# Performance work log

Hardware: AMD Instinct MI355X
Metric: run time of the kernel (lower is better)

## Reference

```python
import jax, jax.numpy as jnp
import numpy as np

H = 256
L = 3
LN_EPS = 1e-5


def _layernorm(z, g, b):
    mu = jnp.mean(z, axis=-1, keepdims=True)
    var = jnp.mean(jnp.square(z - mu), axis=-1, keepdims=True)
    return (z - mu) / jnp.sqrt(var + LN_EPS) * g + b


def setup_inputs() -> dict:
    key = jax.random.key(0)
    ks = jax.random.split(key, 32)
    B, n = 32, 1024
    N = B * n
    E = 16 * N
    node_in, edge_in = 3, 4
    s = 0.05
    inp = {
        'x': jax.random.normal(ks[0], (N, node_in), jnp.float32),
        'edge_attr': jax.random.normal(ks[1], (E, edge_in), jnp.float32),
        'edge_index': jax.random.randint(ks[2], (2, E), 0, N, jnp.int64),
        'a': jax.random.randint(ks[3], (B, n), 0, 2, jnp.int32),
        # node_proj: Linear(node_in+1 -> H)
        'np_w': jax.random.normal(ks[4], (node_in + 1, H), jnp.float32) * s,
        'np_b': jnp.zeros((H,), jnp.float32),
        # edge_mlp: Linear(edge_in->H), ReLU, Linear(H->H)
        'em_w1': jax.random.normal(ks[5], (edge_in, H), jnp.float32) * s,
        'em_b1': jnp.zeros((H,), jnp.float32),
        'em_w2': jax.random.normal(ks[6], (H, H), jnp.float32) * s,
        'em_b2': jnp.zeros((H,), jnp.float32),
        # per-layer GINEConv internal edge lin (edge_dim=H -> H)
        'lin_w': jax.random.normal(ks[7], (L, H, H), jnp.float32) * s,
        'lin_b': jnp.zeros((L, H), jnp.float32),
        # per-layer GINEConv nn: Linear(H->H), ReLU, Linear(H->H)
        'm_w1': jax.random.normal(ks[8], (L, H, H), jnp.float32) * s,
        'm_b1': jnp.zeros((L, H), jnp.float32),
        'm_w2': jax.random.normal(ks[9], (L, H, H), jnp.float32) * s,
        'm_b2': jnp.zeros((L, H), jnp.float32),
        # per-layer LayerNorm
        'ln_g': jnp.ones((L, H), jnp.float32),
        'ln_b': jnp.zeros((L, H), jnp.float32),
        # head: Linear(H->H), ReLU, Linear(H->1)
        'hd_w1': jax.random.normal(ks[10], (H, H), jnp.float32) * s,
        'hd_b1': jnp.zeros((H,), jnp.float32),
        'hd_w2': jax.random.normal(ks[11], (H, 1), jnp.float32) * s,
        'hd_b2': jnp.zeros((1,), jnp.float32),
    }
    return inp


def reference(x, edge_attr, edge_index, a,
              np_w, np_b, em_w1, em_b1, em_w2, em_b2,
              lin_w, lin_b, m_w1, m_b1, m_w2, m_b2, ln_g, ln_b,
              hd_w1, hd_b1, hd_w2, hd_b2):
    N = x.shape[0]
    B, n = a.shape
    # graphs are packed contiguously: batch = i//n, local = i%n ->
    # a[batch, local] == a.reshape(-1)
    a_s = a.reshape(-1).astype(x.dtype)[:, None]            # [N,1]
    h = jax.nn.relu(jnp.concatenate([x, a_s], -1) @ np_w + np_b)  # [N,H]
    e = jax.nn.relu(edge_attr @ em_w1 + em_b1) @ em_w2 + em_b2    # [E,H]
    src, dst = edge_index[0], edge_index[1]
    for l in range(L):
        e_l = e @ lin_w[l] + lin_b[l]                       # GINEConv edge lin
        msg = jax.nn.relu(h[src] + e_l)                     # [E,H]
        agg = jax.ops.segment_sum(msg, dst, num_segments=N) # scatter-add
        z = h + agg                                          # (1+eps)*h, eps=0
        z = jax.nn.relu(z @ m_w1[l] + m_b1[l]) @ m_w2[l] + m_b2[l]
        z = _layernorm(z, ln_g[l], ln_b[l])
        h = h + jax.nn.relu(z)                              # residual
    batch_vec = jnp.arange(N) // n
    g = jax.ops.segment_sum(h, batch_vec, num_segments=B) / n  # mean pool
    q = (jax.nn.relu(g @ hd_w1 + hd_b1) @ hd_w2 + hd_b2)[:, 0]
    return q
```

## Files before the change

kernel.cpp:

```cpp
#include <hip/hip_runtime.h>
#include <hip/hip_bf16.h>

#define H 256
#define LN_EPS 1e-5f
#define PITCH 264
#define TE 128

typedef __attribute__((ext_vector_type(8))) short bf16x8;
typedef __attribute__((ext_vector_type(4))) float f32x4;

__device__ __forceinline__ float bf2f(unsigned short u) {
  union { unsigned int i; float f; } v; v.i = ((unsigned int)u) << 16; return v.f;
}
__device__ __forceinline__ unsigned short f2bf(float f) {
  union { float f; unsigned int i; } v; v.f = f;
  unsigned int x = v.i;
  return (unsigned short)((x + 0x7fffu + ((x >> 16) & 1u)) >> 16);
}
__device__ __forceinline__ unsigned int pack2bf(float a, float b) {
  __hip_bfloat162 t = __float22bfloat162_rn(make_float2(a, b));
  unsigned int u;
  __builtin_memcpy(&u, &t, 4);
  return u;
}
__device__ __forceinline__ unsigned short f2bf1(float a) {
  return (unsigned short)pack2bf(a, a);
}
__device__ __forceinline__ void fsplit(float v, unsigned short& hi, unsigned short& lo) {
  hi = f2bf(v);
  lo = f2bf(v - bf2f(hi));
}

__device__ __forceinline__ void gemm_tile(const float* __restrict__ sA,
                                          const float* __restrict__ W,
                                          int lane_j, int rg, float acc[8][4]) {
#pragma unroll
  for (int mm = 0; mm < 8; mm++)
#pragma unroll
    for (int cc = 0; cc < 4; cc++) acc[mm][cc] = 0.f;
  for (int k = 0; k < H; k += 4) {
    float tvf[8][4];
#pragma unroll
    for (int mm = 0; mm < 8; mm++)
      *(float4*)&tvf[mm][0] = *(const float4*)&sA[(rg * 8 + mm) * H + k];
#pragma unroll
    for (int kk = 0; kk < 4; kk++) {
      const float* wr = W + (k + kk) * H + lane_j;
      float w0 = wr[0], w1 = wr[64], w2 = wr[128], w3 = wr[192];
#pragma unroll
      for (int mm = 0; mm < 8; mm++) {
        float av = tvf[mm][kk];
        acc[mm][0] = fmaf(av, w0, acc[mm][0]);
        acc[mm][1] = fmaf(av, w1, acc[mm][1]);
        acc[mm][2] = fmaf(av, w2, acc[mm][2]);
        acc[mm][3] = fmaf(av, w3, acc[mm][3]);
      }
    }
  }
}


__global__ void k_detect(const int* __restrict__ ei, int* __restrict__ flag) {
  if (threadIdx.x == 0 && blockIdx.x == 0)
    *flag = (ei[1] == 0 && ei[3] == 0 && ei[5] == 0 && ei[7] == 0) ? 1 : 0;
}

__global__ __launch_bounds__(256) void k_zero(float4* __restrict__ p, int n4) {
  int i = blockIdx.x * 256 + threadIdx.x;
  if (i < n4) p[i] = make_float4(0.f, 0.f, 0.f, 0.f);
}

__global__ __launch_bounds__(256) void k_hist(
    const void* __restrict__ ei, const int* __restrict__ flag64,
    int* __restrict__ hist, int E) {
  int e = blockIdx.x * 256 + threadIdx.x;
  if (e >= E) return;
  int d = (*flag64) ? (int)((const long long*)ei)[(size_t)E + e]
                    : ((const int*)ei)[(size_t)E + e];
  atomicAdd(&hist[d], 1);
}

__global__ __launch_bounds__(256) void k_scan(
    const int* __restrict__ hist, int* __restrict__ cursor, int N) {
  __shared__ int part[256];
  int tid = threadIdx.x;
  int chunk = (N + 255) / 256;
  int s = 0;
  for (int i = 0; i < chunk; i++) {
    int idx = tid * chunk + i;
    if (idx < N) s += hist[idx];
  }
  part[tid] = s;
  __syncthreads();
  for (int off = 1; off < 256; off <<= 1) {
    int v = (tid >= off) ? part[tid - off] : 0;
    __syncthreads();
    part[tid] += v;
    __syncthreads();
  }
  int excl = (tid == 0) ? 0 : part[tid - 1];
  for (int i = 0; i < chunk; i++) {
    int idx = tid * chunk + i;
    if (idx < N) {
      cursor[idx] = excl;
      excl += hist[idx];
    }
  }
}

__global__ __launch_bounds__(256) void k_scatter(
    const void* __restrict__ ei, const int* __restrict__ flag64,
    const float* __restrict__ ea, int* __restrict__ cursor,
    int* __restrict__ srcS, int* __restrict__ dstS, float* __restrict__ eaS, int E) {
  int e = blockIdx.x * 256 + threadIdx.x;
  if (e >= E) return;
  int is64 = *flag64;
  int s = is64 ? (int)((const long long*)ei)[e] : ((const int*)ei)[e];
  int d = is64 ? (int)((const long long*)ei)[(size_t)E + e]
               : ((const int*)ei)[(size_t)E + e];
  int p = atomicAdd(&cursor[d], 1);
  srcS[p] = s;
  dstS[p] = d;
  ((float4*)eaS)[p] = ((const float4*)ea)[e];
}

__global__ __launch_bounds__(256) void k_node_proj(
    const float* __restrict__ x, const int* __restrict__ a,
    const float* __restrict__ w, const float* __restrict__ b,
    float* __restrict__ h, int N) {
  int node = blockIdx.x;
  int j = threadIdx.x;
  float acc = b[j];
  acc = fmaf(x[node * 3 + 0], w[0 * H + j], acc);
  acc = fmaf(x[node * 3 + 1], w[1 * H + j], acc);
  acc = fmaf(x[node * 3 + 2], w[2 * H + j], acc);
  acc = fmaf((float)a[node], w[3 * H + j], acc);
  h[(size_t)node * H + j] = fmaxf(acc, 0.f);
}

__global__ __launch_bounds__(256, 2) void k_wcomb(
    const float* __restrict__ w2, const float* __restrict__ lin_w,
    unsigned short* __restrict__ wcTh, unsigned short* __restrict__ wcTl) {
  __shared__ __align__(16) float sA[32 * H];
  int l = blockIdx.x >> 3, tile = blockIdx.x & 7;
  int tid = threadIdx.x;
  const float4* src = (const float4*)(w2 + (size_t)tile * 32 * H);
#pragma unroll
  for (int it = 0; it < 8; it++) {
    int vi = it * 256 + tid;
    *(float4*)&sA[vi * 4] = src[vi];
  }
  __syncthreads();
  int lane_j = tid & 63, rg = tid >> 6;
  float acc[8][4];
  gemm_tile(sA, lin_w + (size_t)l * H * H, lane_j, rg, acc);
  unsigned short* oh = wcTh + (size_t)l * H * H;
  unsigned short* ol = wcTl + (size_t)l * H * H;
#pragma unroll
  for (int cc = 0; cc < 4; cc++) {
    int j = lane_j + 64 * cc;
#pragma unroll
    for (int mm = 0; mm < 8; mm++) {
      int k = tile * 32 + rg * 8 + mm;
      unsigned short hi, lo;
      fsplit(acc[mm][cc], hi, lo);
      oh[(size_t)j * H + k] = hi;
      ol[(size_t)j * H + k] = lo;
    }
  }
}

__global__ __launch_bounds__(256) void k_beta(
    const float* __restrict__ lin_w, const float* __restrict__ lin_b,
    const float* __restrict__ b2, float* __restrict__ beta) {
  int l = blockIdx.x, j = threadIdx.x;
  const float* W = lin_w + (size_t)l * H * H;
  float v = lin_b[l * H + j];
  for (int k = 0; k < H; k++) v = fmaf(b2[k], W[k * H + j], v);
  beta[l * H + j] = v;
}

__global__ __launch_bounds__(256) void k_transp(
    const float* __restrict__ in,
    unsigned short* __restrict__ outh, unsigned short* __restrict__ outl) {
  int l = blockIdx.z;
  int kb = blockIdx.x * 64, nb = blockIdx.y * 64;
  int tid = threadIdx.x;
  __shared__ float T[64][65];
  const float* src = in + (size_t)l * H * H;
#pragma unroll
  for (int it = 0; it < 16; it++) {
    int idx = it * 256 + tid;
    int kl = idx >> 6, nl = idx & 63;
    T[kl][nl] = src[(size_t)(kb + kl) * H + nb + nl];
  }
  __syncthreads();
  unsigned short* dh = outh + (size_t)l * H * H;
  unsigned short* dl = outl + (size_t)l * H * H;
#pragma unroll
  for (int it = 0; it < 8; it++) {
    int u = it * 256 + tid;
    int nl = u >> 5, k2 = (u & 31) * 2;
    unsigned short h0, l0, h1, l1;
    fsplit(T[k2][nl], h0, l0);
    fsplit(T[k2 + 1][nl], h1, l1);
    size_t o = (size_t)(nb + nl) * H + kb + k2;
    *(unsigned int*)&dh[o] = (unsigned int)h0 | ((unsigned int)h1 << 16);
    *(unsigned int*)&dl[o] = (unsigned int)l0 | ((unsigned int)l1 << 16);
  }
}


__global__ __launch_bounds__(1024, 8) void k_edge_mfma(
    const float* __restrict__ eaS,
    const float* __restrict__ w1, const float* __restrict__ b1,
    const unsigned short* __restrict__ Wth,
    const float* __restrict__ beta,
    const float* __restrict__ h, float* __restrict__ agg,
    const int* __restrict__ srcS, const int* __restrict__ dstS) {
  __shared__ __align__(16) unsigned short sAh[TE * PITCH];
  __shared__ __align__(16) float sEA[TE * 4];
  __shared__ int sSrc[TE];
  __shared__ int sDst[TE];
  int tid = threadIdx.x;
  int base = blockIdx.x * TE;
  if (tid < TE) {
    sSrc[tid] = srcS[base + tid];
  } else if (tid < 2 * TE) {
    sDst[tid - TE] = dstS[base + tid - TE];
  } else if (tid < 3 * TE) {
    int t = tid - 2 * TE;
    ((float4*)sEA)[t] = ((const float4*)(eaS + (size_t)base * 4))[t];
  }
  __syncthreads();
  {
    int j2 = (tid & 127) * 2;
    int r0 = (tid >> 7) * 16;
    float wv0[4], wv1[4];
#pragma unroll
    for (int q = 0; q < 4; q++) { wv0[q] = w1[q * H + j2]; wv1[q] = w1[q * H + j2 + 1]; }
    float bb0 = b1[j2], bb1 = b1[j2 + 1];
#pragma unroll
    for (int m = r0; m < r0 + 16; m++) {
      float t0 = bb0, t1 = bb1;
#pragma unroll
      for (int q = 0; q < 4; q++) {
        float eav = sEA[m * 4 + q];
        t0 = fmaf(eav, wv0[q], t0);
        t1 = fmaf(eav, wv1[q], t1);
      }
      *(unsigned int*)&sAh[m * PITCH + j2] = pack2bf(fmaxf(t0, 0.f), fmaxf(t1, 0.f));
    }
  }
  __syncthreads();
  int lane = tid & 63, wv = tid >> 6;
  int lane15 = lane & 15, quad = lane >> 4;
  f32x4 acc[8];
#pragma unroll
  for (int i = 0; i < 8; i++) acc[i] = (f32x4){0.f, 0.f, 0.f, 0.f};
  const unsigned short* aph = sAh + lane15 * PITCH + quad * 8;
  const unsigned short* bph = Wth + (size_t)(wv * 16 + lane15) * H + quad * 8;
#pragma unroll
  for (int st = 0; st < 8; st++) {
    bf16x8 bhf = *(const bf16x8*)(bph + st * 32);
#pragma unroll
    for (int rg = 0; rg < 8; rg++) {
      bf16x8 ah = *(const bf16x8*)(aph + rg * 16 * PITCH + st * 32);
      acc[rg] = __builtin_amdgcn_mfma_f32_16x16x32_bf16(ah, bhf, acc[rg], 0, 0, 0);
    }
  }
  float bv = beta[wv * 16 + lane15];
  __syncthreads();
#pragma unroll
  for (int rg = 0; rg < 8; rg++) {
#pragma unroll
    for (int r = 0; r < 4; r++) {
      int row = rg * 16 + quad * 4 + r;
      sAh[row * PITCH + wv * 16 + lane15] = f2bf1(acc[rg][r] + bv);
    }
  }
  int jcol = tid & 255, quarter = tid >> 8;
  const int* msrc = sSrc + quarter * 32;
  unsigned int hvp[16];
#pragma unroll
  for (int p = 0; p < 16; p++) {
    float f0 = h[(size_t)msrc[2 * p] * H + jcol];
    float f1 = h[(size_t)msrc[2 * p + 1] * H + jcol];
    hvp[p] = pack2bf(f0, f1);
  }
  __syncthreads();
  {
    const int* mdst = sDst + quarter * 32;
    float run = 0.f;
    int prev = mdst[0];
#pragma unroll
    for (int m = 0; m < 32; m++) {
      int d = mdst[m];
      unsigned int hp = hvp[m >> 1];
      unsigned short hu = (m & 1) ? (unsigned short)(hp >> 16) : (unsigned short)hp;
      float msg = fmaxf(bf2f(hu) + bf2f(sAh[(quarter * 32 + m) * PITCH + jcol]), 0.f);
      if (d != prev) {
        atomicAdd(&agg[(size_t)prev * H + jcol], run);
        run = 0.f;
        prev = d;
      }
      run += msg;
    }
    atomicAdd(&agg[(size_t)prev * H + jcol], run);
  }
}

__global__ __launch_bounds__(256) void k_node_mfma(
    float* __restrict__ h, const float* __restrict__ agg,
    const unsigned short* __restrict__ w1Th, const float* __restrict__ b1,
    const unsigned short* __restrict__ w2Th, const float* __restrict__ b2,
    const float* __restrict__ lng, const float* __restrict__ lnb) {
  __shared__ __align__(16) unsigned short sAh[32 * PITCH];
  __shared__ float sPartS[32][4];
  __shared__ float sPartQ[32][4];
  __shared__ float sMu[32];
  __shared__ float sRstd[32];
  int tid = threadIdx.x;
  int base = blockIdx.x * 32;
  const float4* h4 = (const float4*)(h + (size_t)base * H);
  const float4* a4 = (const float4*)(agg + (size_t)base * H);
#pragma unroll
  for (int it = 0; it < 8; it++) {
    int vi = it * 256 + tid;
    int row = vi >> 6, c4 = (vi & 63) * 4;
    float4 hv = h4[vi], av = a4[vi];
    uint2 uh;
    uh.x = pack2bf(hv.x + av.x, hv.y + av.y);
    uh.y = pack2bf(hv.z + av.z, hv.w + av.w);
    *(uint2*)&sAh[row * PITCH + c4] = uh;
  }
  __syncthreads();
  int lane = tid & 63, wv = tid >> 6;
  int lane15 = lane & 15, quad = lane >> 4;
  int col0 = wv * 64;
  const unsigned short* aph = sAh + lane15 * PITCH + quad * 8;
  f32x4 acc[2][4];
#pragma unroll
  for (int i = 0; i < 2; i++)
#pragma unroll
    for (int c = 0; c < 4; c++) acc[i][c] = (f32x4){0.f, 0.f, 0.f, 0.f};
  {
    const unsigned short* bph = w1Th + (size_t)(col0 + lane15) * H + quad * 8;
#pragma unroll
    for (int st = 0; st < 8; st++) {
      bf16x8 ah[2];
#pragma unroll
      for (int rg = 0; rg < 2; rg++)
        ah[rg] = *(const bf16x8*)(aph + rg * 16 * PITCH + st * 32);
#pragma unroll
      for (int cl = 0; cl < 4; cl++) {
        bf16x8 bhf = *(const bf16x8*)(bph + (size_t)cl * 16 * H + st * 32);
#pragma unroll
        for (int rg = 0; rg < 2; rg++)
          acc[rg][cl] = __builtin_amdgcn_mfma_f32_16x16x32_bf16(ah[rg], bhf, acc[rg][cl], 0, 0, 0);
      }
    }
  }
  float b1v[4];
#pragma unroll
  for (int cl = 0; cl < 4; cl++) b1v[cl] = b1[col0 + cl * 16 + lane15];
  __syncthreads();
#pragma unroll
  for (int rg = 0; rg < 2; rg++)
#pragma unroll
    for (int r = 0; r < 4; r++) {
      int row = rg * 16 + quad * 4 + r;
#pragma unroll
      for (int cl = 0; cl < 4; cl++) {
        int col = col0 + cl * 16 + lane15;
        sAh[row * PITCH + col] = f2bf1(fmaxf(acc[rg][cl][r] + b1v[cl], 0.f));
      }
    }
  __syncthreads();
  f32x4 acc2[2][4];
#pragma unroll
  for (int i = 0; i < 2; i++)
#pragma unroll
    for (int c = 0; c < 4; c++) acc2[i][c] = (f32x4){0.f, 0.f, 0.f, 0.f};
  {
    const unsigned short* bph = w2Th + (size_t)(col0 + lane15) * H + quad * 8;
#pragma unroll
    for (int st = 0; st < 8; st++) {
      bf16x8 ah[2];
#pragma unroll
      for (int rg = 0; rg < 2; rg++)
        ah[rg] = *(const bf16x8*)(aph + rg * 16 * PITCH + st * 32);
#pragma unroll
      for (int cl = 0; cl < 4; cl++) {
        bf16x8 bhf = *(const bf16x8*)(bph + (size_t)cl * 16 * H + st * 32);
#pragma unroll
        for (int rg = 0; rg < 2; rg++)
          acc2[rg][cl] = __builtin_amdgcn_mfma_f32_16x16x32_bf16(ah[rg], bhf, acc2[rg][cl], 0, 0, 0);
      }
    }
  }
  float b2v[4], gv[4], bbv[4];
#pragma unroll
  for (int cl = 0; cl < 4; cl++) {
    int col = col0 + cl * 16 + lane15;
    b2v[cl] = b2[col]; gv[cl] = lng[col]; bbv[cl] = lnb[col];
  }
#pragma unroll
  for (int rg = 0; rg < 2; rg++)
#pragma unroll
    for (int r = 0; r < 4; r++) {
      int row = rg * 16 + quad * 4 + r;
      float s = 0.f, ss = 0.f;
#pragma unroll
      for (int cl = 0; cl < 4; cl++) {
        float z2 = acc2[rg][cl][r] + b2v[cl];
        s += z2;
        ss = fmaf(z2, z2, ss);
      }
      s += __shfl_xor(s, 1, 64); ss += __shfl_xor(ss, 1, 64);
      s += __shfl_xor(s, 2, 64); ss += __shfl_xor(ss, 2, 64);
      s += __shfl_xor(s, 4, 64); ss += __shfl_xor(ss, 4, 64);
      s += __shfl_xor(s, 8, 64); ss += __shfl_xor(ss, 8, 64);
      if (lane15 == 0) { sPartS[row][wv] = s; sPartQ[row][wv] = ss; }
    }
  __syncthreads();
  if (tid < 32) {
    float s = sPartS[tid][0] + sPartS[tid][1] + sPartS[tid][2] + sPartS[tid][3];
    float ss = sPartQ[tid][0] + sPartQ[tid][1] + sPartQ[tid][2] + sPartQ[tid][3];
    float mu = s * (1.f / H);
    float var = ss * (1.f / H) - mu * mu;
    sMu[tid] = mu;
    sRstd[tid] = rsqrtf(var + LN_EPS);
  }
  __syncthreads();
#pragma unroll
  for (int rg = 0; rg < 2; rg++)
#pragma unroll
    for (int r = 0; r < 4; r++) {
      int row = rg * 16 + quad * 4 + r;
      float mu = sMu[row], rstd = sRstd[row];
      float* hr = h + (size_t)(base + row) * H;
#pragma unroll
      for (int cl = 0; cl < 4; cl++) {
        int col = col0 + cl * 16 + lane15;
        float z2 = acc2[rg][cl][r] + b2v[cl];
        float v = fmaf((z2 - mu) * rstd, gv[cl], bbv[cl]);
        hr[col] = hr[col] + fmaxf(v, 0.f);
      }
    }
}

__global__ __launch_bounds__(256) void k_pool(
    const float* __restrict__ h, float* __restrict__ g, int n) {
  int tid = threadIdx.x;
  int row0 = blockIdx.x * 64;
  int b = row0 / n;
  const float* hb = h + (size_t)row0 * H;
  float s0 = 0.f, s1 = 0.f, s2 = 0.f, s3 = 0.f;
  for (int i = 0; i < 64; i += 4) {
    s0 += hb[(size_t)(i + 0) * H + tid];
    s1 += hb[(size_t)(i + 1) * H + tid];
    s2 += hb[(size_t)(i + 2) * H + tid];
    s3 += hb[(size_t)(i + 3) * H + tid];
  }
  atomicAdd(&g[(size_t)b * H + tid], s0 + s1 + s2 + s3);
}

__global__ __launch_bounds__(256) void k_head(
    const float* __restrict__ g,
    const float* __restrict__ w1, const float* __restrict__ b1,
    const float* __restrict__ w2, const float* __restrict__ b2,
    float* __restrict__ out, int n) {
  __shared__ float sG[H];
  __shared__ float sT[H];
  __shared__ float sR[4];
  int b = blockIdx.x, tid = threadIdx.x;
  sG[tid] = g[(size_t)b * H + tid] / (float)n;
  __syncthreads();
  float t = b1[tid];
  for (int k = 0; k < H; k++) t = fmaf(sG[k], w1[k * H + tid], t);
  sT[tid] = fmaxf(t, 0.f);
  __syncthreads();
  float p = sT[tid] * w2[tid];
#pragma unroll
  for (int off = 32; off > 0; off >>= 1) p += __shfl_xor(p, off, 64);
  if ((tid & 63) == 0) sR[tid >> 6] = p;
  __syncthreads();
  if (tid == 0) out[b] = sR[0] + sR[1] + sR[2] + sR[3] + b2[0];
}

extern "C" void kernel_launch(void* const* d_in, const int* in_sizes, int n_in,
                              void* d_out, int out_size, void* d_ws, size_t ws_size,
                              hipStream_t stream) {
  const float* x      = (const float*)d_in[0];
  const float* ea     = (const float*)d_in[1];
  const void*  ei     = d_in[2];
  const int*   a      = (const int*)d_in[3];
  const float* np_w   = (const float*)d_in[4];
  const float* np_b   = (const float*)d_in[5];
  const float* em_w1  = (const float*)d_in[6];
  const float* em_b1  = (const float*)d_in[7];
  const float* em_w2  = (const float*)d_in[8];
  const float* em_b2  = (const float*)d_in[9];
  const float* lin_w  = (const float*)d_in[10];
  const float* lin_b  = (const float*)d_in[11];
  const float* m_w1   = (const float*)d_in[12];
  const float* m_b1   = (const float*)d_in[13];
  const float* m_w2   = (const float*)d_in[14];
  const float* m_b2   = (const float*)d_in[15];
  const float* ln_g   = (const float*)d_in[16];
  const float* ln_b   = (const float*)d_in[17];
  const float* hd_w1  = (const float*)d_in[18];
  const float* hd_b1  = (const float*)d_in[19];
  const float* hd_w2  = (const float*)d_in[20];
  const float* hd_b2  = (const float*)d_in[21];

  int N = in_sizes[0] / 3;
  int E = in_sizes[1] / 4;
  int B = out_size;
  int n = N / B;

  char* ws = (char*)d_ws;
  size_t off = 0;
  auto alloc = [&](size_t bytes) {
    char* p = ws + off;
    off += (bytes + 255) & ~(size_t)255;
    return p;
  };
  float* h    = (float*)alloc((size_t)N * H * 4);
  float* agg  = (float*)alloc((size_t)N * H * 4);
  unsigned short* wcTh = (unsigned short*)alloc((size_t)3 * H * H * 2);
  unsigned short* wcTl = (unsigned short*)alloc((size_t)3 * H * H * 2);
  unsigned short* w1Th = (unsigned short*)alloc((size_t)3 * H * H * 2);
  unsigned short* w1Tl = (unsigned short*)alloc((size_t)3 * H * H * 2);
  unsigned short* w2Th = (unsigned short*)alloc((size_t)3 * H * H * 2);
  unsigned short* w2Tl = (unsigned short*)alloc((size_t)3 * H * H * 2);
  float* beta  = (float*)alloc(3 * H * 4);
  int*   flag  = (int*)alloc(4);
  int*   hist  = (int*)alloc((size_t)N * 4);
  int*   curs  = (int*)alloc((size_t)N * 4);
  int*   srcS  = (int*)alloc((size_t)E * 4);
  int*   dstS  = (int*)alloc((size_t)E * 4);
  float* eaS   = (float*)alloc((size_t)E * 4 * 4);
  float* g     = (float*)alloc((size_t)B * H * 4);

  float* out = (float*)d_out;
  int ebl = (E + 255) / 256;

  k_detect<<<1, 64, 0, stream>>>((const int*)ei, flag);
  k_zero<<<(N + 1023) / 1024, 256, 0, stream>>>((float4*)hist, N / 4);
  k_hist<<<ebl, 256, 0, stream>>>(ei, flag, hist, E);
  k_scan<<<1, 256, 0, stream>>>(hist, curs, N);
  k_scatter<<<ebl, 256, 0, stream>>>(ei, flag, ea, curs, srcS, dstS, eaS, E);
  k_node_proj<<<N, 256, 0, stream>>>(x, a, np_w, np_b, h, N);
  k_wcomb<<<24, 256, 0, stream>>>(em_w2, lin_w, wcTh, wcTl);
  k_beta<<<3, 256, 0, stream>>>(lin_w, lin_b, em_b2, beta);
  k_transp<<<dim3(4, 4, 3), 256, 0, stream>>>(m_w1, w1Th, w1Tl);
  k_transp<<<dim3(4, 4, 3), 256, 0, stream>>>(m_w2, w2Th, w2Tl);

  int n4 = N * H / 4;
  for (int l = 0; l < 3; l++) {
    k_zero<<<(n4 + 255) / 256, 256, 0, stream>>>((float4*)agg, n4);
    k_edge_mfma<<<E / TE, 1024, 0, stream>>>(eaS, em_w1, em_b1,
                                             wcTh + (size_t)l * H * H,
                                             beta + (size_t)l * H,
                                             h, agg, srcS, dstS);
    k_node_mfma<<<N / 32, 256, 0, stream>>>(h, agg,
                                            w1Th + (size_t)l * H * H,
                                            m_b1 + (size_t)l * H,
                                            w2Th + (size_t)l * H * H,
                                            m_b2 + (size_t)l * H,
                                            ln_g + (size_t)l * H, ln_b + (size_t)l * H);
  }
  int g4 = B * H / 4;
  k_zero<<<(g4 + 255) / 256, 256, 0, stream>>>((float4*)g, g4);
  k_pool<<<N / 64, 256, 0, stream>>>(h, g, n);
  k_head<<<B, 256, 0, stream>>>(g, hd_w1, hd_b1, hd_w2, hd_b2, out, n);
}
```

Before: 889.0 us.

## Keep a bf16 shadow copy of h for edge gathers; retile node kernel to 64 rows

Node kernels now also write a bf16 copy of the hidden state, and the edge kernel gathers h[src] from that copy instead of loading fp32 and packing it. This halves the bytes moved by the random gather that dominates the edge kernel. The node MLP kernel is retiled to 64 rows per block with 1024 threads, where each wave owns 16 output columns, with a 16-way partial LayerNorm reduction. The cost is an extra bf16 store per node per layer and a different MFMA and occupancy profile in the node kernel.

```diff
diff --git a/kernel.cpp b/kernel.cpp
--- a/kernel.cpp
+++ b/kernel.cpp
@@ -127,7 +127,7 @@
 __global__ __launch_bounds__(256) void k_node_proj(
     const float* __restrict__ x, const int* __restrict__ a,
     const float* __restrict__ w, const float* __restrict__ b,
-    float* __restrict__ h, int N) {
+    float* __restrict__ h, unsigned short* __restrict__ hbf, int N) {
   int node = blockIdx.x;
   int j = threadIdx.x;
   float acc = b[j];
@@ -135,7 +135,9 @@
   acc = fmaf(x[node * 3 + 1], w[1 * H + j], acc);
   acc = fmaf(x[node * 3 + 2], w[2 * H + j], acc);
   acc = fmaf((float)a[node], w[3 * H + j], acc);
-  h[(size_t)node * H + j] = fmaxf(acc, 0.f);
+  float v = fmaxf(acc, 0.f);
+  h[(size_t)node * H + j] = v;
+  hbf[(size_t)node * H + j] = f2bf1(v);
 }
 
 __global__ __launch_bounds__(256, 2) void k_wcomb(
@@ -216,7 +218,7 @@
     const float* __restrict__ w1, const float* __restrict__ b1,
     const unsigned short* __restrict__ Wth,
     const float* __restrict__ beta,
-    const float* __restrict__ h, float* __restrict__ agg,
+    const unsigned short* __restrict__ hbf, float* __restrict__ agg,
     const int* __restrict__ srcS, const int* __restrict__ dstS) {
   __shared__ __align__(16) unsigned short sAh[TE * PITCH];
   __shared__ __align__(16) float sEA[TE * 4];
@@ -284,9 +286,9 @@
   unsigned int hvp[16];
 #pragma unroll
   for (int p = 0; p < 16; p++) {
-    float f0 = h[(size_t)msrc[2 * p] * H + jcol];
-    float f1 = h[(size_t)msrc[2 * p + 1] * H + jcol];
-    hvp[p] = pack2bf(f0, f1);
+    unsigned int u0 = hbf[(size_t)msrc[2 * p] * H + jcol];
+    unsigned int u1 = hbf[(size_t)msrc[2 * p + 1] * H + jcol];
+    hvp[p] = u0 | (u1 << 16);
   }
   __syncthreads();
   {
@@ -310,23 +312,24 @@
   }
 }
 
-__global__ __launch_bounds__(256) void k_node_mfma(
-    float* __restrict__ h, const float* __restrict__ agg,
+__global__ __launch_bounds__(1024, 8) void k_node_mfma(
+    float* __restrict__ h, unsigned short* __restrict__ hbf,
+    const float* __restrict__ agg,
     const unsigned short* __restrict__ w1Th, const float* __restrict__ b1,
     const unsigned short* __restrict__ w2Th, const float* __restrict__ b2,
     const float* __restrict__ lng, const float* __restrict__ lnb) {
-  __shared__ __align__(16) unsigned short sAh[32 * PITCH];
-  __shared__ float sPartS[32][4];
-  __shared__ float sPartQ[32][4];
-  __shared__ float sMu[32];
-  __shared__ float sRstd[32];
+  __shared__ __align__(16) unsigned short sAh[64 * PITCH];
+  __shared__ float sPartS[64][16];
+  __shared__ float sPartQ[64][16];
+  __shared__ float sMu[64];
+  __shared__ float sRstd[64];
   int tid = threadIdx.x;
-  int base = blockIdx.x * 32;
+  int base = blockIdx.x * 64;
   const float4* h4 = (const float4*)(h + (size_t)base * H);
   const float4* a4 = (const float4*)(agg + (size_t)base * H);
 #pragma unroll
-  for (int it = 0; it < 8; it++) {
-    int vi = it * 256 + tid;
+  for (int it = 0; it < 4; it++) {
+    int vi = it * 1024 + tid;
     int row = vi >> 6, c4 = (vi & 63) * 4;
     float4 hv = h4[vi], av = a4[vi];
     uint2 uh;
@@ -337,86 +340,56 @@
   __syncthreads();
   int lane = tid & 63, wv = tid >> 6;
   int lane15 = lane & 15, quad = lane >> 4;
-  int col0 = wv * 64;
+  int col = wv * 16 + lane15;
   const unsigned short* aph = sAh + lane15 * PITCH + quad * 8;
-  f32x4 acc[2][4];
-#pragma unroll
-  for (int i = 0; i < 2; i++)
-#pragma unroll
-    for (int c = 0; c < 4; c++) acc[i][c] = (f32x4){0.f, 0.f, 0.f, 0.f};
+  f32x4 acc[4];
+#pragma unroll
+  for (int i = 0; i < 4; i++) acc[i] = (f32x4){0.f, 0.f, 0.f, 0.f};
   {
-    const unsigned short* bph = w1Th + (size_t)(col0 + lane15) * H + quad * 8;
+    const unsigned short* bph = w1Th + (size_t)col * H + quad * 8;
 #pragma unroll
     for (int st = 0; st < 8; st++) {
-      bf16x8 ah[2];
-#pragma unroll
-      for (int rg = 0; rg < 2; rg++)
-        ah[rg] = *(const bf16x8*)(aph + rg * 16 * PITCH + st * 32);
-#pragma unroll
-      for (int cl = 0; cl < 4; cl++) {
-        bf16x8 bhf = *(const bf16x8*)(bph + (size_t)cl * 16 * H + st * 32);
-#pragma unroll
-        for (int rg = 0; rg < 2; rg++)
-          acc[rg][cl] = __builtin_amdgcn_mfma_f32_16x16x32_bf16(ah[rg], bhf, acc[rg][cl], 0, 0, 0);
+      bf16x8 bhf = *(const bf16x8*)(bph + st * 32);
+#pragma unroll
+      for (int rg = 0; rg < 4; rg++) {
+        bf16x8 ah = *(const bf16x8*)(aph + rg * 16 * PITCH + st * 32);
+        acc[rg] = __builtin_amdgcn_mfma_f32_16x16x32_bf16(ah, bhf, acc[rg], 0, 0, 0);
       }
     }
   }
-  float b1v[4];
-#pragma unroll
-  for (int cl = 0; cl < 4; cl++) b1v[cl] = b1[col0 + cl * 16 + lane15];
-  __syncthreads();
-#pragma unroll
-  for (int rg = 0; rg < 2; rg++)
+  float b1v = b1[col];
+  __syncthreads();
+#pragma unroll
+  for (int rg = 0; rg < 4; rg++)
 #pragma unroll
     for (int r = 0; r < 4; r++) {
       int row = rg * 16 + quad * 4 + r;
-#pragma unroll
-      for (int cl = 0; cl < 4; cl++) {
-        int col = col0 + cl * 16 + lane15;
-        sAh[row * PITCH + col] = f2bf1(fmaxf(acc[rg][cl][r] + b1v[cl], 0.f));
+      sAh[row * PITCH + col] = f2bf1(fmaxf(acc[rg][r] + b1v, 0.f));
+    }
+  __syncthreads();
+  f32x4 acc2[4];
+#pragma unroll
+  for (int i = 0; i < 4; i++) acc2[i] = (f32x4){0.f, 0.f, 0.f, 0.f};
+  {
+    const unsigned short* bph = w2Th + (size_t)col * H + quad * 8;
+#pragma unroll
+    for (int st = 0; st < 8; st++) {
+      bf16x8 bhf = *(const bf16x8*)(bph + st * 32);
+#pragma unroll
+      for (int rg = 0; rg < 4; rg++) {
+        bf16x8 ah = *(const bf16x8*)(aph + rg * 16 * PITCH + st * 32);
+        acc2[rg] = __builtin_amdgcn_mfma_f32_16x16x32_bf16(ah, bhf, acc2[rg], 0, 0, 0);
       }
     }
-  __syncthreads();
-  f32x4 acc2[2][4];
-#pragma unroll
-  for (int i = 0; i < 2; i++)
-#pragma unroll
-    for (int c = 0; c < 4; c++) acc2[i][c] = (f32x4){0.f, 0.f, 0.f, 0.f};
-  {
-    const unsigned short* bph = w2Th + (size_t)(col0 + lane15) * H + quad * 8;
-#pragma unroll
-    for (int st = 0; st < 8; st++) {
-      bf16x8 ah[2];
-#pragma unroll
-      for (int rg = 0; rg < 2; rg++)
-        ah[rg] = *(const bf16x8*)(aph + rg * 16 * PITCH + st * 32);
-#pragma unroll
-      for (int cl = 0; cl < 4; cl++) {
-        bf16x8 bhf = *(const bf16x8*)(bph + (size_t)cl * 16 * H + st * 32);
-#pragma unroll
-        for (int rg = 0; rg < 2; rg++)
-          acc2[rg][cl] = __builtin_amdgcn_mfma_f32_16x16x32_bf16(ah[rg], bhf, acc2[rg][cl], 0, 0, 0);
-      }
-    }
-  }
-  float b2v[4], gv[4], bbv[4];
-#pragma unroll
-  for (int cl = 0; cl < 4; cl++) {
-    int col = col0 + cl * 16 + lane15;
-    b2v[cl] = b2[col]; gv[cl] = lng[col]; bbv[cl] = lnb[col];
-  }
-#pragma unroll
-  for (int rg = 0; rg < 2; rg++)
+  }
+  float b2v = b2[col], gv = lng[col], bbv = lnb[col];
+#pragma unroll
+  for (int rg = 0; rg < 4; rg++)
 #pragma unroll
     for (int r = 0; r < 4; r++) {
       int row = rg * 16 + quad * 4 + r;
-      float s = 0.f, ss = 0.f;
-#pragma unroll
-      for (int cl = 0; cl < 4; cl++) {
-        float z2 = acc2[rg][cl][r] + b2v[cl];
-        s += z2;
-        ss = fmaf(z2, z2, ss);
-      }
+      float z2 = acc2[rg][r] + b2v;
+      float s = z2, ss = z2 * z2;
       s += __shfl_xor(s, 1, 64); ss += __shfl_xor(ss, 1, 64);
       s += __shfl_xor(s, 2, 64); ss += __shfl_xor(ss, 2, 64);
       s += __shfl_xor(s, 4, 64); ss += __shfl_xor(ss, 4, 64);
@@ -424,9 +397,10 @@
       if (lane15 == 0) { sPartS[row][wv] = s; sPartQ[row][wv] = ss; }
     }
   __syncthreads();
-  if (tid < 32) {
-    float s = sPartS[tid][0] + sPartS[tid][1] + sPartS[tid][2] + sPartS[tid][3];
-    float ss = sPartQ[tid][0] + sPartQ[tid][1] + sPartQ[tid][2] + sPartQ[tid][3];
+  if (tid < 64) {
+    float s = 0.f, ss = 0.f;
+#pragma unroll
+    for (int w = 0; w < 16; w++) { s += sPartS[tid][w]; ss += sPartQ[tid][w]; }
     float mu = s * (1.f / H);
     float var = ss * (1.f / H) - mu * mu;
     sMu[tid] = mu;
@@ -434,19 +408,17 @@
   }
   __syncthreads();
 #pragma unroll
-  for (int rg = 0; rg < 2; rg++)
+  for (int rg = 0; rg < 4; rg++)
 #pragma unroll
     for (int r = 0; r < 4; r++) {
       int row = rg * 16 + quad * 4 + r;
       float mu = sMu[row], rstd = sRstd[row];
-      float* hr = h + (size_t)(base + row) * H;
-#pragma unroll
-      for (int cl = 0; cl < 4; cl++) {
-        int col = col0 + cl * 16 + lane15;
-        float z2 = acc2[rg][cl][r] + b2v[cl];
-        float v = fmaf((z2 - mu) * rstd, gv[cl], bbv[cl]);
-        hr[col] = hr[col] + fmaxf(v, 0.f);
-      }
+      size_t o = (size_t)(base + row) * H + col;
+      float z2 = acc2[rg][r] + b2v;
+      float v = fmaf((z2 - mu) * rstd, gv, bbv);
+      float hn = h[o] + fmaxf(v, 0.f);
+      h[o] = hn;
+      hbf[o] = f2bf1(hn);
     }
 }
 
@@ -528,6 +500,7 @@
     return p;
   };
   float* h    = (float*)alloc((size_t)N * H * 4);
+  unsigned short* hbf = (unsigned short*)alloc((size_t)N * H * 2);
   float* agg  = (float*)alloc((size_t)N * H * 4);
   unsigned short* wcTh = (unsigned short*)alloc((size_t)3 * H * H * 2);
   unsigned short* wcTl = (unsigned short*)alloc((size_t)3 * H * H * 2);
@@ -552,7 +525,7 @@
   k_hist<<<ebl, 256, 0, stream>>>(ei, flag, hist, E);
   k_scan<<<1, 256, 0, stream>>>(hist, curs, N);
   k_scatter<<<ebl, 256, 0, stream>>>(ei, flag, ea, curs, srcS, dstS, eaS, E);
-  k_node_proj<<<N, 256, 0, stream>>>(x, a, np_w, np_b, h, N);
+  k_node_proj<<<N, 256, 0, stream>>>(x, a, np_w, np_b, h, hbf, N);
   k_wcomb<<<24, 256, 0, stream>>>(em_w2, lin_w, wcTh, wcTl);
   k_beta<<<3, 256, 0, stream>>>(lin_w, lin_b, em_b2, beta);
   k_transp<<<dim3(4, 4, 3), 256, 0, stream>>>(m_w1, w1Th, w1Tl);
@@ -564,13 +537,13 @@
     k_edge_mfma<<<E / TE, 1024, 0, stream>>>(eaS, em_w1, em_b1,
                                              wcTh + (size_t)l * H * H,
                                              beta + (size_t)l * H,
-                                             h, agg, srcS, dstS);
-    k_node_mfma<<<N / 32, 256, 0, stream>>>(h, agg,
-                                            w1Th + (size_t)l * H * H,
-                                            m_b1 + (size_t)l * H,
-                                            w2Th + (size_t)l * H * H,
-                                            m_b2 + (size_t)l * H,
-                                            ln_g + (size_t)l * H, ln_b + (size_t)l * H);
+                                             hbf, agg, srcS, dstS);
+    k_node_mfma<<<N / 64, 1024, 0, stream>>>(h, hbf, agg,
+                                             w1Th + (size_t)l * H * H,
+                                             m_b1 + (size_t)l * H,
+                                             w2Th + (size_t)l * H * H,
+                                             m_b2 + (size_t)l * H,
+                                             ln_g + (size_t)l * H, ln_b + (size_t)l * H);
   }
   int g4 = B * H / 4;
   k_zero<<<(g4 + 255) / 256, 256, 0, stream>>>((float4*)g, g4);
```

Result: faster. 856.9 us (-3.6%).
